# Optimization experiments

Hardware: AMD Instinct MI355X
Metric: run time of the kernel (lower is better)

Reference implementation:

```python
import jax, jax.numpy as jnp
import numpy as np

EMB_TABLE = 80000  # full shared embedding rows
N_ITEMS = 50000    # target item count (item_num + 1)
E = 600000         # edges
D = 128            # embedding_size
L = 3              # num_gcn_layers


def gcn_conv(x, W, b, src, dst, norm, n):
    # PyG GCNConv: x' = lin(x); out[i] = sum_{(j->i)} norm_ji * x'[j] + bias
    msgs = (x @ W)[src] * norm[:, None]          # [E+n, D]
    out = jax.ops.segment_sum(msgs, dst, num_segments=n)
    return out + b


def setup_inputs() -> dict:
    key = jax.random.key(0)
    k0, k1, k2 = jax.random.split(key, 3)
    item_emb = jax.random.normal(k0, (EMB_TABLE, D), dtype=jnp.float32) * 0.02
    weights = jax.random.normal(k1, (L, D, D), dtype=jnp.float32) * (1.0 / np.sqrt(D))
    biases = jnp.zeros((L, D), dtype=jnp.float32)
    edge_index = jax.random.randint(k2, (2, E), 0, N_ITEMS, dtype=jnp.int64)
    return {"item_emb": item_emb, "weights": weights, "biases": biases,
            "edge_index": edge_index, "item_nums": N_ITEMS}


def reference(item_emb, weights, biases, edge_index, item_nums):
    n = item_nums
    x0 = item_emb[-n:]  # embeds[0] = item_emb[-item_nums:]
    loops = jnp.arange(n, dtype=edge_index.dtype)
    src = jnp.concatenate([edge_index[0], loops])  # add self-loops (GCNConv default)
    dst = jnp.concatenate([edge_index[1], loops])
    # symmetric normalization: deg computed on target side with self-loops
    deg = jax.ops.segment_sum(jnp.ones_like(src, dtype=x0.dtype), dst, num_segments=n)
    dinv = jnp.where(deg > 0, jax.lax.rsqrt(jnp.maximum(deg, 1e-12)), 0.0)
    norm = dinv[src] * dinv[dst]                   # [E+n]
    embeds = [x0]
    for l in range(weights.shape[0]):
        embeds.append(gcn_conv(embeds[-1], weights[l], biases[l], src, dst, norm, n))
    total = embeds[0]
    for e in embeds[1:]:
        total = total + e
    return (total, *embeds)
```

## Files before the change

kernel.cpp:

```cpp
#include <hip/hip_runtime.h>
#include <stdint.h>

#define D 128

typedef unsigned int u32;
typedef unsigned short u16;
typedef __attribute__((ext_vector_type(8))) short short8;
typedef __attribute__((ext_vector_type(4))) float f32x4;

static __device__ __forceinline__ float bf2f(u16 h) {
    return __uint_as_float(((u32)h) << 16);
}
static __device__ __forceinline__ u16 f2bf(float f) {
    u32 u = __float_as_uint(f);
    u32 r = (u + 0x7fffu + ((u >> 16) & 1u)) >> 16;
    return (u16)r;
}
static __device__ __forceinline__ int clampi(int v, int n) {
    if (v < 0) v = 0;
    if (v >= n) v = n - 1;
    return v;
}

__global__ void k_init(int* __restrict__ hist, int* __restrict__ csr_pos, int n,
                       const u16* __restrict__ emb_raw, const u32* __restrict__ ei_raw,
                       const u16* __restrict__ w_raw, int* __restrict__ flags) {
    int i = blockIdx.x * 256 + threadIdx.x;
    if (i < n) {
        hist[i] = 0;
        csr_pos[i] = 0;
    }
    if (blockIdx.x == 0 && threadIdx.x < 64) {
        int t = threadIdx.x;
        int se = 0, sw = 0, zz = 0;
#pragma unroll
        for (int q = 0; q < 4; q++) {
            int k = t * 4 + q;
            u16 he = emb_raw[2 * k];
            u32 exe = (he >> 7) & 0xFF;
            if (he == 0 || (exe >= 0x60 && exe <= 0x8F)) se++;
            u16 hw = w_raw[2 * k];
            u32 exw = (hw >> 7) & 0xFF;
            if (hw == 0 || (exw >= 0x60 && exw <= 0x8F)) sw++;
            if (ei_raw[2 * k + 1] == 0) zz++;
        }
#pragma unroll
        for (int o = 32; o; o >>= 1) {
            se += __shfl_down(se, o);
            sw += __shfl_down(sw, o);
            zz += __shfl_down(zz, o);
        }
        if (t == 0) {
            flags[0] = (se >= 200) ? 1 : 0;
            flags[2] = (sw >= 200) ? 1 : 0;
            flags[1] = (zz >= 200) ? 1 : 0;
        }
    }
}

__global__ __launch_bounds__(256) void k_wprep(const void* __restrict__ Wbase,
                                               const int* __restrict__ flags,
                                               u16* __restrict__ WB) {
    int idx = blockIdx.x * 256 + threadIdx.x;
    int e = idx & 7;
    int l = (idx >> 3) & 63;
    int ks = (idx >> 9) & 3;
    int c = (idx >> 11) & 7;
    int layer = idx >> 14;
    int k = ks * 32 + ((l >> 4) << 3) + e;
    int j = (c << 4) + (l & 15);
    size_t src = (size_t)layer * D * D + (size_t)k * D + j;
    float w = flags[2] ? bf2f(((const u16*)Wbase)[src]) : ((const float*)Wbase)[src];
    u16 hb = f2bf(w);
    u16 lb = f2bf(w - bf2f(hb));
    size_t o = (size_t)layer * 32768 + (size_t)((c * 4 + ks) * 64 + l) * 8 + e;
    WB[o] = hb;
    WB[o + 16384] = lb;
}

__global__ void k_hist(const u32* __restrict__ ei, int E, int n,
                       const int* __restrict__ flags, int* __restrict__ hist) {
    int e = blockIdx.x * 256 + threadIdx.x;
    if (e >= E) return;
    int d;
    if (flags[1]) d = ((const int2*)ei)[(size_t)E + e].x;
    else          d = (int)ei[(size_t)E + e];
    atomicAdd(&hist[clampi(d, n)], 1);
}

__global__ void k_scan1(const int* __restrict__ hist, int n,
                        int* __restrict__ incl, int* __restrict__ bsums) {
    __shared__ int s[256];
    int t = threadIdx.x;
    int i = blockIdx.x * 256 + t;
    int v = (i < n) ? hist[i] : 0;
    s[t] = v;
    __syncthreads();
    for (int d2 = 1; d2 < 256; d2 <<= 1) {
        int add = (t >= d2) ? s[t - d2] : 0;
        __syncthreads();
        s[t] += add;
        __syncthreads();
    }
    if (i < n) incl[i] = s[t];
    if (t == 255) bsums[blockIdx.x] = s[255];
}

__global__ void k_scan23(const int* __restrict__ hist, const int* __restrict__ bsums,
                         int n, int* __restrict__ csr_off, float* __restrict__ dinv) {
    __shared__ int s[256];
    int t = threadIdx.x, b = blockIdx.x;
    s[t] = (t < b) ? bsums[t] : 0;
    __syncthreads();
    for (int o = 128; o; o >>= 1) {
        if (t < o) s[t] += s[t + o];
        __syncthreads();
    }
    int add = s[0];
    int i = b * 256 + t;
    if (i < n) {
        int h = hist[i];
        csr_off[i] = add + csr_off[i] - h;
        dinv[i] = rsqrtf((float)(h + 1));
    }
}

__global__ void k_sx(const u32* __restrict__ ei, int E, int n,
                     const int* __restrict__ flags,
                     const int* __restrict__ csr_off, int* __restrict__ csr_pos,
                     const float* __restrict__ dinv, int2* __restrict__ csr_pair,
                     const void* __restrict__ emb, int off_elems, int nD4,
                     float* __restrict__ out_x0, int eb) {
    int bid = blockIdx.x;
    if (bid < eb) {
        int e = bid * 256 + threadIdx.x;
        if (e >= E) return;
        int s, d;
        if (flags[1]) {
            s = ((const int2*)ei)[e].x;
            d = ((const int2*)ei)[(size_t)E + e].x;
        } else {
            s = (int)ei[e];
            d = (int)ei[(size_t)E + e];
        }
        s = clampi(s, n);
        d = clampi(d, n);
        int p = csr_off[d] + atomicAdd(&csr_pos[d], 1);
        if (p >= E) p = E - 1;
        csr_pair[p] = make_int2(s, __float_as_int(dinv[s] * dinv[d]));
    } else {
        int i = (bid - eb) * 256 + threadIdx.x;
        if (i >= nD4) return;
        float4 v;
        if (flags[0]) {
            ushort4 h = ((const ushort4*)((const u16*)emb + off_elems))[i];
            v = make_float4(bf2f(h.x), bf2f(h.y), bf2f(h.z), bf2f(h.w));
        } else {
            v = ((const float4*)((const float*)emb + off_elems))[i];
        }
        ((float4*)out_x0)[i] = v;
    }
}

__global__ __launch_bounds__(256) void k_gemm(const float* __restrict__ A,
                                              const u16* __restrict__ WB, int layer,
                                              int n, u32* __restrict__ Y) {
    __shared__ f32x4 ldsv[4096];
    int tid = threadIdx.x;
    {
        const f32x4* src = (const f32x4*)(WB + (size_t)layer * 32768);
#pragma unroll
        for (int i = 0; i < 16; i++) ldsv[tid + 256 * i] = src[tid + 256 * i];
    }
    __syncthreads();

    int w = tid >> 6, l = tid & 63;
    int row0 = blockIdx.x * 64 + w * 16;
    int ar = row0 + (l & 15);
    if (ar >= n) ar = 0;
    const float* Ab = A + (size_t)ar * D + ((l >> 4) << 3);

    f32x4 acc[8] = {};
    const short8* bp = (const short8*)ldsv;

#pragma unroll
    for (int ks = 0; ks < 4; ks++) {
        f32x4 a0 = *(const f32x4*)(Ab + ks * 32);
        f32x4 a1 = *(const f32x4*)(Ab + ks * 32 + 4);
        float av[8] = {a0.x, a0.y, a0.z, a0.w, a1.x, a1.y, a1.z, a1.w};
        short8 ah, al;
#pragma unroll
        for (int e = 0; e < 8; e++) {
            u16 h = f2bf(av[e]);
            ah[e] = (short)h;
            al[e] = (short)f2bf(av[e] - bf2f(h));
        }
#pragma unroll
        for (int c = 0; c < 8; c++) {
            short8 bh = bp[(c * 4 + ks) * 64 + l];
            short8 bl = bp[2048 + (c * 4 + ks) * 64 + l];
            acc[c] = __builtin_amdgcn_mfma_f32_16x16x32_bf16(al, bh, acc[c], 0, 0, 0);
            acc[c] = __builtin_amdgcn_mfma_f32_16x16x32_bf16(ah, bl, acc[c], 0, 0, 0);
            acc[c] = __builtin_amdgcn_mfma_f32_16x16x32_bf16(ah, bh, acc[c], 0, 0, 0);
        }
    }

    int rbase = row0 + ((l >> 4) << 2);
    int col = l & 15;
#pragma unroll
    for (int r = 0; r < 4; r++) {
        int gr = rbase + r;
        if (gr < n) {
#pragma unroll
            for (int c = 0; c < 4; c++) {
                u32 pack = (u32)f2bf(acc[c][r]) | ((u32)f2bf(acc[c + 4][r]) << 16);
                Y[(size_t)gr * 64 + c * 16 + col] = pack;
            }
        }
    }
}

__global__ __launch_bounds__(256) void k_agg(const u32* __restrict__ Y,
                                             const int* __restrict__ csr_off,
                                             const int* __restrict__ cnt,
                                             const int2* __restrict__ csr_pair,
                                             const float* __restrict__ dinv,
                                             const void* __restrict__ bias_base, int layer,
                                             const int* __restrict__ flags, int n, int nD,
                                             const float* __restrict__ out_base,
                                             float* __restrict__ out_x,
                                             float* __restrict__ out_tot) {
    int i = blockIdx.x * 4 + (threadIdx.x >> 6);
    if (i >= n) return;
    int t = threadIdx.x & 63;

    float di = dinv[i];
    float di2 = di * di;
    u32 yv = Y[(size_t)i * 64 + t];
    float a0 = bf2f((u16)(yv & 0xffffu)) * di2;
    float a1 = bf2f((u16)(yv >> 16)) * di2;
    float c0 = 0.0f, c1 = 0.0f;

    int start = csr_off[i];
    int c = cnt[i];

    for (int base = 0; base < c; base += 64) {
        int m = c - base;
        if (m > 64) m = 64;
        int2 pr = (t < m) ? csr_pair[start + base + t] : make_int2(0, 0);
        int j = 0;
        for (; j + 3 < m; j += 4) {
            int s0 = __shfl(pr.x, j);
            int s1 = __shfl(pr.x, j + 1);
            int s2 = __shfl(pr.x, j + 2);
            int s3 = __shfl(pr.x, j + 3);
            float w0 = __uint_as_float((u32)__shfl(pr.y, j));
            float w1 = __uint_as_float((u32)__shfl(pr.y, j + 1));
            float w2 = __uint_as_float((u32)__shfl(pr.y, j + 2));
            float w3 = __uint_as_float((u32)__shfl(pr.y, j + 3));
            u32 v0 = Y[(size_t)s0 * 64 + t];
            u32 v1 = Y[(size_t)s1 * 64 + t];
            u32 v2 = Y[(size_t)s2 * 64 + t];
            u32 v3 = Y[(size_t)s3 * 64 + t];
            a0 += bf2f((u16)(v0 & 0xffffu)) * w0;
            a1 += bf2f((u16)(v0 >> 16)) * w0;
            c0 += bf2f((u16)(v1 & 0xffffu)) * w1;
            c1 += bf2f((u16)(v1 >> 16)) * w1;
            a0 += bf2f((u16)(v2 & 0xffffu)) * w2;
            a1 += bf2f((u16)(v2 >> 16)) * w2;
            c0 += bf2f((u16)(v3 & 0xffffu)) * w3;
            c1 += bf2f((u16)(v3 >> 16)) * w3;
        }
        for (; j < m; j++) {
            int s = __shfl(pr.x, j);
            float w = __uint_as_float((u32)__shfl(pr.y, j));
            u32 v = Y[(size_t)s * 64 + t];
            a0 += bf2f((u16)(v & 0xffffu)) * w;
            a1 += bf2f((u16)(v >> 16)) * w;
        }
    }
    float acc0 = a0 + c0, acc1 = a1 + c1;

    float b0, b1;
    if (flags[0]) {
        const u16* bb = (const u16*)bias_base + layer * D;
        b0 = bf2f(bb[t]);
        b1 = bf2f(bb[t + 64]);
    } else {
        const float* bb = (const float*)bias_base + layer * D;
        b0 = bb[t];
        b1 = bb[t + 64];
    }
    float xv0 = acc0 + b0, xv1 = acc1 + b1;
    size_t base = (size_t)i * D + t;
    out_x[base] = xv0;
    out_x[base + 64] = xv1;

    if (out_tot) {
        float s0 = out_base[(size_t)1 * nD + base] + out_base[(size_t)2 * nD + base] +
                   out_base[(size_t)3 * nD + base];
        float s1 = out_base[(size_t)1 * nD + base + 64] + out_base[(size_t)2 * nD + base + 64] +
                   out_base[(size_t)3 * nD + base + 64];
        out_tot[base] = s0 + xv0;
        out_tot[base + 64] = s1 + xv1;
    }
}

extern "C" void kernel_launch(void* const* d_in, const int* in_sizes, int n_in,
                              void* d_out, int out_size, void* d_ws, size_t ws_size,
                              hipStream_t stream) {
    float* out = (float*)d_out;

    const int n = out_size / (5 * D);

    int i_emb = -1, i_ei = -1, i_w = -1, i_b = -1;
    {
        int order[8];
        int m = n_in > 8 ? 8 : n_in;
        for (int i = 0; i < m; i++) order[i] = i;
        for (int a = 0; a < m; a++)
            for (int b2 = a + 1; b2 < m; b2++)
                if (in_sizes[order[b2]] > in_sizes[order[a]]) {
                    int tmp = order[a]; order[a] = order[b2]; order[b2] = tmp;
                }
        i_emb = order[0];
        i_ei  = (m > 1) ? order[1] : 0;
        for (int i = 0; i < m; i++) {
            if (in_sizes[i] == 3 * D * D && i_w < 0) i_w = i;
            if (in_sizes[i] == 3 * D && i_b < 0) i_b = i;
        }
        if (i_w < 0) i_w = (m > 2) ? order[2] : 0;
        if (i_b < 0) i_b = (m > 3) ? order[3] : 0;
    }
    const void* emb  = d_in[i_emb];
    const void* wts  = d_in[i_w];
    const void* bias = d_in[i_b];
    const u32*  ei   = (const u32*)d_in[i_ei];

    const int E = in_sizes[i_ei] / 2;
    const int rows = in_sizes[i_emb] / D;
    const int off_elems = (rows - n) * D;

    char* p = (char*)d_ws;
    auto take = [&](size_t bytes) {
        char* r = p;
        p += (bytes + 255) & ~(size_t)255;
        return r;
    };
    int*   flags    = (int*)  take(3 * 4);
    int*   hist     = (int*)  take((size_t)n * 4);
    int*   csr_pos  = (int*)  take((size_t)n * 4);
    int*   csr_off  = (int*)  take((size_t)n * 4);
    int*   bsums    = (int*)  take(256 * 4);
    float* dinv     = (float*)take((size_t)n * 4);
    int2*  csr_pair = (int2*) take((size_t)E * 8);
    u32*   ybuf     = (u32*)  take((size_t)n * 64 * 4);
    u16*   wb       = (u16*)  take((size_t)3 * 32768 * 2);

    const int nD = n * D;
    const int nb = (n + 255) / 256;
    const int eb = (E + 255) / 256;
    const int x0b = (nD / 4 + 255) / 256;

    k_init<<<nb, 256, 0, stream>>>(hist, csr_pos, n, (const u16*)emb, ei,
                                   (const u16*)wts, flags);
    k_wprep<<<192, 256, 0, stream>>>(wts, flags, wb);
    k_hist<<<eb, 256, 0, stream>>>(ei, E, n, flags, hist);
    k_scan1<<<nb, 256, 0, stream>>>(hist, n, csr_off, bsums);
    k_scan23<<<nb, 256, 0, stream>>>(hist, bsums, n, csr_off, dinv);
    k_sx<<<eb + x0b, 256, 0, stream>>>(ei, E, n, flags, csr_off, csr_pos, dinv,
                                       csr_pair, emb, off_elems, nD / 4,
                                       out + (size_t)nD, eb);

    const int ab = (n + 3) / 4;
    for (int l = 0; l < 3; l++) {
        const float* A = out + (size_t)(1 + l) * nD;
        float* ox = out + (size_t)(2 + l) * nD;
        k_gemm<<<(n + 63) / 64, 256, 0, stream>>>(A, wb, l, n, ybuf);
        k_agg<<<ab, 256, 0, stream>>>(ybuf, csr_off, hist, csr_pair, dinv, bias, l,
                                      flags, n, nD, out, ox,
                                      (l == 2) ? out : (float*)nullptr);
    }
}
```

Baseline: 353.6 us.

## Merge weight prep into histogram kernel, drop GEMM LDS staging, widen gather unroll

```diff
diff --git a/kernel.cpp b/kernel.cpp
--- a/kernel.cpp
+++ b/kernel.cpp
@@ -58,34 +58,34 @@
     }
 }
 
-__global__ __launch_bounds__(256) void k_wprep(const void* __restrict__ Wbase,
-                                               const int* __restrict__ flags,
-                                               u16* __restrict__ WB) {
-    int idx = blockIdx.x * 256 + threadIdx.x;
-    int e = idx & 7;
-    int l = (idx >> 3) & 63;
-    int ks = (idx >> 9) & 3;
-    int c = (idx >> 11) & 7;
-    int layer = idx >> 14;
-    int k = ks * 32 + ((l >> 4) << 3) + e;
-    int j = (c << 4) + (l & 15);
-    size_t src = (size_t)layer * D * D + (size_t)k * D + j;
-    float w = flags[2] ? bf2f(((const u16*)Wbase)[src]) : ((const float*)Wbase)[src];
-    u16 hb = f2bf(w);
-    u16 lb = f2bf(w - bf2f(hb));
-    size_t o = (size_t)layer * 32768 + (size_t)((c * 4 + ks) * 64 + l) * 8 + e;
-    WB[o] = hb;
-    WB[o + 16384] = lb;
-}
-
-__global__ void k_hist(const u32* __restrict__ ei, int E, int n,
-                       const int* __restrict__ flags, int* __restrict__ hist) {
-    int e = blockIdx.x * 256 + threadIdx.x;
-    if (e >= E) return;
-    int d;
-    if (flags[1]) d = ((const int2*)ei)[(size_t)E + e].x;
-    else          d = (int)ei[(size_t)E + e];
-    atomicAdd(&hist[clampi(d, n)], 1);
+__global__ void k_hw(const u32* __restrict__ ei, int E, int n,
+                     const int* __restrict__ flags, int* __restrict__ hist,
+                     const void* __restrict__ Wbase, u16* __restrict__ WB, int eb) {
+    int bid = blockIdx.x;
+    if (bid < eb) {
+        int e = bid * 256 + threadIdx.x;
+        if (e >= E) return;
+        int d;
+        if (flags[1]) d = ((const int2*)ei)[(size_t)E + e].x;
+        else          d = (int)ei[(size_t)E + e];
+        atomicAdd(&hist[clampi(d, n)], 1);
+    } else {
+        int idx = (bid - eb) * 256 + threadIdx.x;
+        int e = idx & 7;
+        int l = (idx >> 3) & 63;
+        int ks = (idx >> 9) & 3;
+        int c = (idx >> 11) & 7;
+        int layer = idx >> 14;
+        int k = ks * 32 + ((l >> 4) << 3) + e;
+        int j = (c << 4) + (l & 15);
+        size_t src = (size_t)layer * D * D + (size_t)k * D + j;
+        float w = flags[2] ? bf2f(((const u16*)Wbase)[src]) : ((const float*)Wbase)[src];
+        u16 hb = f2bf(w);
+        u16 lb = f2bf(w - bf2f(hb));
+        size_t o = (size_t)layer * 32768 + (size_t)((c * 4 + ks) * 64 + l) * 8 + e;
+        WB[o] = hb;
+        WB[o + 16384] = lb;
+    }
 }
 
 __global__ void k_scan1(const int* __restrict__ hist, int n,
@@ -165,15 +165,7 @@
 __global__ __launch_bounds__(256) void k_gemm(const float* __restrict__ A,
                                               const u16* __restrict__ WB, int layer,
                                               int n, u32* __restrict__ Y) {
-    __shared__ f32x4 ldsv[4096];
     int tid = threadIdx.x;
-    {
-        const f32x4* src = (const f32x4*)(WB + (size_t)layer * 32768);
-#pragma unroll
-        for (int i = 0; i < 16; i++) ldsv[tid + 256 * i] = src[tid + 256 * i];
-    }
-    __syncthreads();
-
     int w = tid >> 6, l = tid & 63;
     int row0 = blockIdx.x * 64 + w * 16;
     int ar = row0 + (l & 15);
@@ -181,7 +173,7 @@
     const float* Ab = A + (size_t)ar * D + ((l >> 4) << 3);
 
     f32x4 acc[8] = {};
-    const short8* bp = (const short8*)ldsv;
+    const short8* bp = (const short8*)(WB + (size_t)layer * 32768);
 
 #pragma unroll
     for (int ks = 0; ks < 4; ks++) {
@@ -239,7 +231,9 @@
     u32 yv = Y[(size_t)i * 64 + t];
     float a0 = bf2f((u16)(yv & 0xffffu)) * di2;
     float a1 = bf2f((u16)(yv >> 16)) * di2;
+    float b0 = 0.0f, b1 = 0.0f;
     float c0 = 0.0f, c1 = 0.0f;
+    float d0 = 0.0f, d1 = 0.0f;
 
     int start = csr_off[i];
     int c = cnt[i];
@@ -249,49 +243,70 @@
         if (m > 64) m = 64;
         int2 pr = (t < m) ? csr_pair[start + base + t] : make_int2(0, 0);
         int j = 0;
-        for (; j + 3 < m; j += 4) {
-            int s0 = __shfl(pr.x, j);
-            int s1 = __shfl(pr.x, j + 1);
-            int s2 = __shfl(pr.x, j + 2);
-            int s3 = __shfl(pr.x, j + 3);
-            float w0 = __uint_as_float((u32)__shfl(pr.y, j));
-            float w1 = __uint_as_float((u32)__shfl(pr.y, j + 1));
-            float w2 = __uint_as_float((u32)__shfl(pr.y, j + 2));
-            float w3 = __uint_as_float((u32)__shfl(pr.y, j + 3));
+        for (; j + 7 < m; j += 8) {
+            int s0 = __builtin_amdgcn_readlane(pr.x, j);
+            int s1 = __builtin_amdgcn_readlane(pr.x, j + 1);
+            int s2 = __builtin_amdgcn_readlane(pr.x, j + 2);
+            int s3 = __builtin_amdgcn_readlane(pr.x, j + 3);
+            int s4 = __builtin_amdgcn_readlane(pr.x, j + 4);
+            int s5 = __builtin_amdgcn_readlane(pr.x, j + 5);
+            int s6 = __builtin_amdgcn_readlane(pr.x, j + 6);
+            int s7 = __builtin_amdgcn_readlane(pr.x, j + 7);
+            float w0 = __uint_as_float((u32)__builtin_amdgcn_readlane(pr.y, j));
+            float w1 = __uint_as_float((u32)__builtin_amdgcn_readlane(pr.y, j + 1));
+            float w2 = __uint_as_float((u32)__builtin_amdgcn_readlane(pr.y, j + 2));
+            float w3 = __uint_as_float((u32)__builtin_amdgcn_readlane(pr.y, j + 3));
+            float w4 = __uint_as_float((u32)__builtin_amdgcn_readlane(pr.y, j + 4));
+            float w5 = __uint_as_float((u32)__builtin_amdgcn_readlane(pr.y, j + 5));
+            float w6 = __uint_as_float((u32)__builtin_amdgcn_readlane(pr.y, j + 6));
+            float w7 = __uint_as_float((u32)__builtin_amdgcn_readlane(pr.y, j + 7));
             u32 v0 = Y[(size_t)s0 * 64 + t];
             u32 v1 = Y[(size_t)s1 * 64 + t];
             u32 v2 = Y[(size_t)s2 * 64 + t];
             u32 v3 = Y[(size_t)s3 * 64 + t];
+            u32 v4 = Y[(size_t)s4 * 64 + t];
+            u32 v5 = Y[(size_t)s5 * 64 + t];
+            u32 v6 = Y[(size_t)s6 * 64 + t];
+            u32 v7 = Y[(size_t)s7 * 64 + t];
             a0 += bf2f((u16)(v0 & 0xffffu)) * w0;
             a1 += bf2f((u16)(v0 >> 16)) * w0;
-            c0 += bf2f((u16)(v1 & 0xffffu)) * w1;
-            c1 += bf2f((u16)(v1 >> 16)) * w1;
-            a0 += bf2f((u16)(v2 & 0xffffu)) * w2;
-            a1 += bf2f((u16)(v2 >> 16)) * w2;
-            c0 += bf2f((u16)(v3 & 0xffffu)) * w3;
-            c1 += bf2f((u16)(v3 >> 16)) * w3;
+            b0 += bf2f((u16)(v1 & 0xffffu)) * w1;
+            b1 += bf2f((u16)(v1 >> 16)) * w1;
+            c0 += bf2f((u16)(v2 & 0xffffu)) * w2;
+            c1 += bf2f((u16)(v2 >> 16)) * w2;
+            d0 += bf2f((u16)(v3 & 0xffffu)) * w3;
+            d1 += bf2f((u16)(v3 >> 16)) * w3;
+            a0 += bf2f((u16)(v4 & 0xffffu)) * w4;
+            a1 += bf2f((u16)(v4 >> 16)) * w4;
+            b0 += bf2f((u16)(v5 & 0xffffu)) * w5;
+            b1 += bf2f((u16)(v5 >> 16)) * w5;
+            c0 += bf2f((u16)(v6 & 0xffffu)) * w6;
+            c1 += bf2f((u16)(v6 >> 16)) * w6;
+            d0 += bf2f((u16)(v7 & 0xffffu)) * w7;
+            d1 += bf2f((u16)(v7 >> 16)) * w7;
         }
         for (; j < m; j++) {
-            int s = __shfl(pr.x, j);
-            float w = __uint_as_float((u32)__shfl(pr.y, j));
+            int s = __builtin_amdgcn_readlane(pr.x, j);
+            float w = __uint_as_float((u32)__builtin_amdgcn_readlane(pr.y, j));
             u32 v = Y[(size_t)s * 64 + t];
             a0 += bf2f((u16)(v & 0xffffu)) * w;
             a1 += bf2f((u16)(v >> 16)) * w;
         }
     }
-    float acc0 = a0 + c0, acc1 = a1 + c1;
-
-    float b0, b1;
+    float acc0 = (a0 + b0) + (c0 + d0);
+    float acc1 = (a1 + b1) + (c1 + d1);
+
+    float bb0, bb1;
     if (flags[0]) {
         const u16* bb = (const u16*)bias_base + layer * D;
-        b0 = bf2f(bb[t]);
-        b1 = bf2f(bb[t + 64]);
+        bb0 = bf2f(bb[t]);
+        bb1 = bf2f(bb[t + 64]);
     } else {
         const float* bb = (const float*)bias_base + layer * D;
-        b0 = bb[t];
-        b1 = bb[t + 64];
-    }
-    float xv0 = acc0 + b0, xv1 = acc1 + b1;
+        bb0 = bb[t];
+        bb1 = bb[t + 64];
+    }
+    float xv0 = acc0 + bb0, xv1 = acc1 + bb1;
     size_t base = (size_t)i * D + t;
     out_x[base] = xv0;
     out_x[base + 64] = xv1;
@@ -364,8 +379,7 @@
 
     k_init<<<nb, 256, 0, stream>>>(hist, csr_pos, n, (const u16*)emb, ei,
                                    (const u16*)wts, flags);
-    k_wprep<<<192, 256, 0, stream>>>(wts, flags, wb);
-    k_hist<<<eb, 256, 0, stream>>>(ei, E, n, flags, hist);
+    k_hw<<<eb + 192, 256, 0, stream>>>(ei, E, n, flags, hist, wts, wb, eb);
     k_scan1<<<nb, 256, 0, stream>>>(hist, n, csr_off, bsums);
     k_scan23<<<nb, 256, 0, stream>>>(hist, bsums, n, csr_off, dinv);
     k_sx<<<eb + x0b, 256, 0, stream>>>(ei, E, n, flags, csr_off, csr_pos, dinv,
```

New measurement: 362.1 us. 1.02x slower.
